# Optimization experiments

Hardware: AMD Instinct MI355X
Metric: run time of the kernel (lower is better)

## Reference

```python
import jax, jax.numpy as jnp
import numpy as np

KS = 3
PAD = 1
N = KS * KS  # 9 sampling points per output location


def setup_inputs() -> dict:
    key = jax.random.key(0)
    k1, k2, k3 = jax.random.split(key, 3)
    b, c, H, W, outc = 4, 128, 64, 64, 128
    x = jax.random.normal(k1, (b, c, H, W), jnp.float32)
    offset = jax.random.normal(k2, (b, 2 * N, H, W), jnp.float32)
    weight = jax.random.normal(k3, (outc, c, KS, KS), jnp.float32) * 0.05
    return {"x": x, "offset": offset, "weight": weight}


def reference(x, offset, weight):
    b, c, H, W = x.shape
    h, w = offset.shape[2], offset.shape[3]
    # reorder interleaved (x,y,x,y,...) offset channels to (all x, all y)
    idx = jnp.concatenate([jnp.arange(0, 2 * N, 2), jnp.arange(1, 2 * N, 2)])
    offset = offset[:, idx]
    # zero padding
    xp = jnp.pad(x, ((0, 0), (0, 0), (PAD, PAD), (PAD, PAD)))
    Hp, Wp = H + 2 * PAD, W + 2 * PAD
    # kernel-relative offsets p_n: [1, 2N, 1, 1]
    r = np.arange(-(KS - 1) // 2, (KS - 1) // 2 + 1)
    pnx, pny = np.meshgrid(r, r, indexing='ij')
    p_n = jnp.asarray(np.concatenate([pnx.flatten(), pny.flatten()]).reshape(1, 2 * N, 1, 1), jnp.float32)
    # base grid p_0: [1, 2N, h, w], coords start at 1 (padded frame)
    p0x, p0y = np.meshgrid(np.arange(1, h + 1), np.arange(1, w + 1), indexing='ij')
    p_0 = jnp.asarray(np.concatenate([np.tile(p0x.reshape(1, 1, h, w), (1, N, 1, 1)),
                                      np.tile(p0y.reshape(1, 1, h, w), (1, N, 1, 1))], axis=1), jnp.float32)
    p = jnp.transpose(p_0 + p_n + offset, (0, 2, 3, 1))  # [b, h, w, 2N]
    px, py = p[..., :N], p[..., N:]
    fx, fy = jnp.floor(px), jnp.floor(py)
    # 4 corner integer coords, clamped to padded image
    q_lt_x = jnp.clip(fx, 0, Hp - 1).astype(jnp.int32)
    q_lt_y = jnp.clip(fy, 0, Wp - 1).astype(jnp.int32)
    q_rb_x = jnp.clip(fx + 1, 0, Hp - 1).astype(jnp.int32)
    q_rb_y = jnp.clip(fy + 1, 0, Wp - 1).astype(jnp.int32)
    # out-of-range mask: snap p to floor(p) there (matches original, incl. zero grad thru floor)
    mask_x = jax.lax.stop_gradient(((px < PAD) | (px > Hp - 1 - PAD)).astype(px.dtype))
    mask_y = jax.lax.stop_gradient(((py < PAD) | (py > Wp - 1 - PAD)).astype(py.dtype))
    px = px * (1 - mask_x) + fx * mask_x
    py = py * (1 - mask_y) + fy * mask_y
    px = jnp.clip(px, 0, Hp - 1)
    py = jnp.clip(py, 0, Wp - 1)
    qltx = q_lt_x.astype(px.dtype); qlty = q_lt_y.astype(px.dtype)
    qrbx = q_rb_x.astype(px.dtype); qrby = q_rb_y.astype(px.dtype)
    # bilinear weights: [b, h, w, N]
    g_lt = (1 + (qltx - px)) * (1 + (qlty - py))
    g_rb = (1 - (qrbx - px)) * (1 - (qrby - py))
    g_lb = (1 + (qltx - px)) * (1 - (qrby - py))
    g_rt = (1 - (qrbx - px)) * (1 + (qlty - py))

    xv = xp.reshape(b, c, Hp * Wp)

    def gather(qx, qy):
        lin = (qx * Wp + qy).reshape(b, 1, h * w * N)
        g = jnp.take_along_axis(xv, jnp.broadcast_to(lin, (b, c, h * w * N)), axis=2)
        return g.reshape(b, c, h, w, N)

    x_off = (g_lt[:, None] * gather(q_lt_x, q_lt_y)
             + g_rb[:, None] * gather(q_rb_x, q_rb_y)
             + g_lb[:, None] * gather(q_lt_x, q_rb_y)
             + g_rt[:, None] * gather(q_rb_x, q_lt_y))  # [b, c, h, w, N]
    # N = i*ks + j -> out[(h,i),(w,j)]
    xo = x_off.reshape(b, c, h, w, KS, KS).transpose(0, 1, 2, 4, 3, 5).reshape(b, c, h * KS, w * KS)
    out = jax.lax.conv_general_dilated(xo, weight, window_strides=(KS, KS), padding='VALID',
                                       dimension_numbers=('NCHW', 'OIHW', 'NCHW'))
    return out
```

## Files before the change

### kernel.cpp

```cpp
#include <hip/hip_runtime.h>


typedef __bf16  v8bf16 __attribute__((ext_vector_type(8)));
typedef __bf16  bf16x2 __attribute__((ext_vector_type(2)));
typedef float   f32x4  __attribute__((ext_vector_type(4)));
typedef float   f32x16 __attribute__((ext_vector_type(16)));
typedef unsigned short ushort4v __attribute__((ext_vector_type(4)));
typedef _Float16 half4v __attribute__((ext_vector_type(4)));

#define CIN  128
#define NPT  9
#define KTOT 1152
#define OC   128
#define PX   32
#define NDESC (NPT * PX)
#define KSTEPS 36
#define KSC  12
#define LDBc 392
#define KS32 72
#define KSC32 24
#define LDR32 392

#define PB_WFRAG 72
#define PB_XPOSE 1024
#define PB_ZERO  2048
#define PB_TOTAL (PB_WFRAG + PB_XPOSE + PB_ZERO)

__device__ __forceinline__ uint4 desc_make(const float* __restrict__ off,
                                           int b, int i, int j, int tap) {
    float ox = off[(((b * 18) + 2 * tap) << 12) + (i << 6) + j];
    float oy = off[(((b * 18) + 2 * tap + 1) << 12) + (i << 6) + j];
    float px = (float)(i + tap / 3) + ox;
    float py = (float)(j + tap % 3) + oy;
    float fx = floorf(px), fy = floorf(py);
    int qltx = (int)fminf(fmaxf(fx, 0.f), 65.f);
    int qlty = (int)fminf(fmaxf(fy, 0.f), 65.f);
    int qrbx = (int)fminf(fmaxf(fx + 1.f, 0.f), 65.f);
    int qrby = (int)fminf(fmaxf(fy + 1.f, 0.f), 65.f);
    if (px < 1.f || px > 64.f) px = fx;
    if (py < 1.f || py > 64.f) py = fy;
    px = fminf(fmaxf(px, 0.f), 65.f);
    py = fminf(fmaxf(py, 0.f), 65.f);
    float wxl = 1.f + (float)qltx - px;
    float wxr = 1.f - ((float)qrbx - px);
    float wyl = 1.f + (float)qlty - py;
    float wyr = 1.f - ((float)qrby - py);
    float g[4] = { wxl * wyl, wxr * wyr, wxl * wyr, wxr * wyl };
    int qx[4] = { qltx, qrbx, qltx, qrbx };
    int qy[4] = { qlty, qrby, qrby, qlty };
    unsigned short idx[4];
    half4v gh;
    #pragma unroll
    for (int cr = 0; cr < 4; ++cr) {
        bool inb = (qx[cr] >= 1) && (qx[cr] <= 64) && (qy[cr] >= 1) && (qy[cr] <= 64);
        idx[cr] = inb ? (unsigned short)((qx[cr] - 1) * 64 + (qy[cr] - 1)) : 0;
        gh[cr]  = inb ? (_Float16)g[cr] : (_Float16)0.f;
    }
    uint4 rec;
    rec.x = (unsigned)idx[0] | ((unsigned)idx[1] << 16);
    rec.y = (unsigned)idx[2] | ((unsigned)idx[3] << 16);
    __builtin_memcpy(&rec.z, &gh, 8);
    return rec;
}

__global__ __launch_bounds__(256) void prep_kernel(
    const float* __restrict__ x, const float* __restrict__ w,
    __bf16* __restrict__ wfrag, __bf16* __restrict__ xt,
    float* __restrict__ out)
{
    __shared__ float tile[64][33];
    const int bid = blockIdx.x;
    const int tid = threadIdx.x;

    if (bid < PB_WFRAG) {
        int t = bid * 256 + tid;
        int lane = t & 63;
        int ks   = (t >> 6) % KS32;
        int ot4  = t / (KS32 * 64);
        int o    = ot4 * 32 + (lane & 31);
        v8bf16 frag;
        #pragma unroll
        for (int e = 0; e < 8; ++e) {
            int k   = ks * 16 + ((lane >> 5) * 8) + e;
            int tap = k >> 7, c = k & 127;
            frag[e] = (__bf16)w[(size_t)o * KTOT + c * NPT + tap];
        }
        *(v8bf16*)(wfrag + (size_t)t * 8) = frag;
    } else if (bid < PB_WFRAG + PB_XPOSE) {
        const int bidx = bid - PB_WFRAG;
        const int b   = bidx >> 8;
        const int hw0 = ((bidx >> 2) & 63) * 64;
        const int c0  = (bidx & 3) * 32;
        #pragma unroll
        for (int r = 0; r < 8; ++r) {
            int c_l  = (tid >> 6) + r * 4;
            int hw_l = tid & 63;
            tile[hw_l][c_l] = x[((size_t)(b * CIN + c0 + c_l) << 12) + hw0 + hw_l];
        }
        __syncthreads();
        #pragma unroll
        for (int r = 0; r < 8; ++r) {
            int hw_l = (tid >> 5) + r * 8;
            int c_l  = tid & 31;
            xt[((size_t)(b * 4096 + hw0 + hw_l)) * CIN + c0 + c_l] = (__bf16)tile[hw_l][c_l];
        }
    } else {
        int t = (bid - PB_WFRAG - PB_XPOSE) * 256 + tid;
        f32x4 z = {0.f, 0.f, 0.f, 0.f};
        *(f32x4*)(out + (size_t)t * 4) = z;
    }
}

__global__ __launch_bounds__(256) void splitk_kernel(
    const float* __restrict__ off, const __bf16* __restrict__ xt,
    const __bf16* __restrict__ wfrag, float* __restrict__ out)
{
    __shared__ __align__(16) __bf16 Bt[PX][LDR32];
    __shared__ __align__(16) uint4 sDesc[96];

    const int bidx = blockIdx.x;
    const int b    = (bidx & 7) >> 1;
    const int sub  = ((bidx >> 3) << 1) | (bidx & 1);
    const int kh3  = sub % 3;
    const int rem  = sub / 3;
    const int i    = rem >> 1;
    const int j0   = (rem & 1) * PX;
    const int tid  = threadIdx.x;

    const int tap0 = kh3 * 3;
    const int l  = tid & 63;
    const int wv = tid >> 6;

    const __bf16* xtb = xt + (((size_t)b << 12) * CIN);

    if (tid < 96) {
        int tt = tid >> 5, p = tid & 31;
        sDesc[tid] = desc_make(off, b, i, j0 + p, tap0 + tt);
    }
    __syncthreads();

    {
        const int q  = l >> 4;
        const int ll = l & 15;
        const __bf16* base = xtb + 8 * ll;

        uint4 qd[6];
        int   pp[6], tt[6];
        #pragma unroll
        for (int m = 0; m < 6; ++m) {
            int dl = wv * 24 + m * 4 + q;
            tt[m] = dl >> 5;
            pp[m] = dl & 31;
            qd[m] = sDesc[dl];
        }

        #pragma unroll
        for (int h = 0; h < 2; ++h) {
            uint4  v[3][4];
            half4v gh[3];
            #pragma unroll
            for (int m = 0; m < 3; ++m) {
                uint4 qm = qd[h * 3 + m];
                unsigned int zz[2] = { qm.z, qm.w };
                __builtin_memcpy(&gh[m], &zz, 8);
                unsigned short idx[4] = {
                    (unsigned short)(qm.x & 0xffff), (unsigned short)(qm.x >> 16),
                    (unsigned short)(qm.y & 0xffff), (unsigned short)(qm.y >> 16) };
                #pragma unroll
                for (int cr = 0; cr < 4; ++cr)
                    v[m][cr] = *(const uint4*)(base + (size_t)idx[cr] * CIN);
            }
            #pragma unroll
            for (int m = 0; m < 3; ++m) {
                float s[8] = {0.f,0.f,0.f,0.f,0.f,0.f,0.f,0.f};
                #pragma unroll
                for (int cr = 0; cr < 4; ++cr) {
                    float gf = (float)gh[m][cr];
                    unsigned int dw[4] = { v[m][cr].x, v[m][cr].y, v[m][cr].z, v[m][cr].w };
                    #pragma unroll
                    for (int e = 0; e < 4; ++e) {
                        float clo, chi;
                        unsigned int lo = dw[e] << 16, hi = dw[e] & 0xffff0000u;
                        __builtin_memcpy(&clo, &lo, 4);
                        __builtin_memcpy(&chi, &hi, 4);
                        s[2 * e]     += gf * clo;
                        s[2 * e + 1] += gf * chi;
                    }
                }
                v8bf16 pr;
                #pragma unroll
                for (int e = 0; e < 8; ++e) pr[e] = (__bf16)s[e];
                int mm = h * 3 + m;
                *(v8bf16*)&Bt[pp[mm]][tt[mm] * CIN + 8 * ll] = pr;
            }
        }
    }
    __syncthreads();

    f32x16 acc = {0.f,0.f,0.f,0.f,0.f,0.f,0.f,0.f,0.f,0.f,0.f,0.f,0.f,0.f,0.f,0.f};
    const __bf16* brow = &Bt[l & 31][(l >> 5) * 8];
    const __bf16* warow = wfrag + (((size_t)wv * KS32 + kh3 * KSC32) * 64 + l) * 8;

    #pragma unroll 6
    for (int ks = 0; ks < KSC32; ++ks) {
        v8bf16 afrag = *(const v8bf16*)(warow + (size_t)ks * 64 * 8);
        v8bf16 bfrag = *(const v8bf16*)(brow + ks * 16);
        acc = __builtin_amdgcn_mfma_f32_32x32x16_bf16(afrag, bfrag, acc, 0, 0, 0);
    }

    {
        int obase = wv * 32 + 4 * (l >> 5);
        float* opb = out + (((size_t)(b * OC + obase)) << 12) + (i << 6) + j0 + (l & 31);
        #pragma unroll
        for (int reg = 0; reg < 16; ++reg) {
            int oo = (reg & 3) + 8 * (reg >> 2);
            unsafeAtomicAdd(opb + ((size_t)oo << 12), acc[reg]);
        }
    }
}

__global__ __launch_bounds__(512, 8) void deform_fused_kernel(
    const float* __restrict__ x, const float* __restrict__ off,
    const float* __restrict__ w, const __bf16* __restrict__ wfrag,
    const __bf16* __restrict__ xt, float* __restrict__ out, int mode)
{
    __shared__ __align__(16) __bf16 Bt[PX][LDBc];
    __shared__ __align__(8)  unsigned short sIdxP[NDESC][4];
    __shared__ __align__(8)  _Float16      sGP[NDESC][4];

    const int bidx = blockIdx.x;
    const int b   = bidx >> 8;
    const int i   = (bidx >> 2) & 63;
    const int j0  = ((bidx >> 1) & 1) * PX;
    const int oh  = bidx & 1;
    const int tid = threadIdx.x;

    if (tid < NDESC) {
        int k = tid >> 5, p = tid & 31;
        int j = j0 + p;
        float ox = off[(((b * 18) + 2 * k) * 64 + i) * 64 + j];
        float oy = off[(((b * 18) + 2 * k + 1) * 64 + i) * 64 + j];
        float px = (float)(i + k / 3) + ox;
        float py = (float)(j + k % 3) + oy;
        float fx = floorf(px), fy = floorf(py);
        int qltx = (int)fminf(fmaxf(fx, 0.f), 65.f);
        int qlty = (int)fminf(fmaxf(fy, 0.f), 65.f);
        int qrbx = (int)fminf(fmaxf(fx + 1.f, 0.f), 65.f);
        int qrby = (int)fminf(fmaxf(fy + 1.f, 0.f), 65.f);
        if (px < 1.f || px > 64.f) px = fx;
        if (py < 1.f || py > 64.f) py = fy;
        px = fminf(fmaxf(px, 0.f), 65.f);
        py = fminf(fmaxf(py, 0.f), 65.f);
        float wxl = 1.f + (float)qltx - px;
        float wxr = 1.f - ((float)qrbx - px);
        float wyl = 1.f + (float)qlty - py;
        float wyr = 1.f - ((float)qrby - py);
        float g[4] = { wxl * wyl, wxr * wyr, wxl * wyr, wxr * wyl };
        int qx[4] = { qltx, qrbx, qltx, qrbx };
        int qy[4] = { qlty, qrby, qrby, qlty };
        #pragma unroll
        for (int cr = 0; cr < 4; ++cr) {
            bool inb = (qx[cr] >= 1) && (qx[cr] <= 64) && (qy[cr] >= 1) && (qy[cr] <= 64);
            sIdxP[tid][cr] = inb ? (unsigned short)((qx[cr] - 1) * 64 + (qy[cr] - 1)) : 0;
            sGP[tid][cr]   = inb ? (_Float16)g[cr] : (_Float16)0.f;
        }
    }
    __syncthreads();

    const int l    = tid & 63;
    const int wv   = tid >> 6;
    const int ot   = oh * 4 + (wv & 3);
    const int ph   = wv >> 2;
    const int quad = l >> 4;
    const int lr   = l & 15;

    f32x4 acc = {0.f, 0.f, 0.f, 0.f};
    const __bf16* xtb = xt + ((size_t)b * 4096) * CIN;
    const float*  xb  = x + ((size_t)b * CIN << 12);
    const __bf16* brow = &Bt[ph * 16 + lr][quad * 8];

    for (int t = 0; t < 3; ++t) {
        if (mode == 2) {
            #pragma unroll 4
            for (int dd = 0; dd < KSC; ++dd) {
                int dl = wv * KSC + dd;
                int tap_l = dl >> 5, p = dl & 31;
                int d = t * 96 + dl;
                ushort4v id = *(const ushort4v*)&sIdxP[d][0];
                half4v   gh = *(const half4v*)&sGP[d][0];
                float s0 = 0.f, s1 = 0.f;
                #pragma unroll
                for (int cr = 0; cr < 4; ++cr) {
                    unsigned int v = *(const unsigned int*)(xtb + (size_t)id[cr] * CIN + 2 * l);
                    float c0v, c1v;
                    unsigned int lo = v << 16, hi = v & 0xffff0000u;
                    __builtin_memcpy(&c0v, &lo, 4);
                    __builtin_memcpy(&c1v, &hi, 4);
                    float gf = (float)gh[cr];
                    s0 += gf * c0v;
                    s1 += gf * c1v;
                }
                bf16x2 pr = { (__bf16)s0, (__bf16)s1 };
                *(bf16x2*)&Bt[p][tap_l * CIN + 2 * l] = pr;
            }
        } else {
            for (int dd = 0; dd < KSC; ++dd) {
                int dl = wv * KSC + dd;
                int tap_l = dl >> 5, p = dl & 31;
                int d = t * 96 + dl;
                ushort4v id = *(const ushort4v*)&sIdxP[d][0];
                half4v   gh = *(const half4v*)&sGP[d][0];
                float s0 = 0.f, s1 = 0.f;
                #pragma unroll
                for (int cr = 0; cr < 4; ++cr) {
                    float gf = (float)gh[cr];
                    s0 += gf * xb[((size_t)(2 * l) << 12) + id[cr]];
                    s1 += gf * xb[((size_t)(2 * l + 1) << 12) + id[cr]];
                }
                bf16x2 pr = { (__bf16)s0, (__bf16)s1 };
                *(bf16x2*)&Bt[p][tap_l * CIN + 2 * l] = pr;
            }
        }
        __syncthreads();

        #pragma unroll 4
        for (int ks = 0; ks < KSC; ++ks) {
            int ks_g = t * KSC + ks;
            v8bf16 bfrag = *(const v8bf16*)(brow + ks * 32);
            v8bf16 afrag;
            if (mode >= 1) {
                afrag = *(const v8bf16*)(wfrag + (((size_t)ot * KSTEPS + ks_g) * 64 + l) * 8);
            } else {
                int o = ot * 16 + lr;
                #pragma unroll
                for (int e = 0; e < 8; ++e) {
                    int k = ks_g * 32 + quad * 8 + e;
                    int tap = k >> 7, c = k & 127;
                    afrag[e] = (__bf16)w[(size_t)o * KTOT + c * NPT + tap];
                }
            }
            acc = __builtin_amdgcn_mfma_f32_16x16x32_bf16(afrag, bfrag, acc, 0, 0, 0);
        }
        if (t < 2) __syncthreads();
    }

    {
        int obase = ot * 16 + quad * 4;
        float* op = out + (((size_t)(b * OC + obase)) << 12) + (i << 6) + j0 + ph * 16 + lr;
        #pragma unroll
        for (int r = 0; r < 4; ++r)
            op[(size_t)r << 12] = acc[r];
    }
}

__global__ __launch_bounds__(256) void wfrag_kernel(const float* __restrict__ w,
                                                    __bf16* __restrict__ wfrag) {
    int t = blockIdx.x * 256 + threadIdx.x;
    if (t >= 8 * KSTEPS * 64) return;
    int lane = t & 63;
    int ks   = (t >> 6) % KSTEPS;
    int ot   = t / (KSTEPS * 64);
    int o    = ot * 16 + (lane & 15);
    v8bf16 frag;
    #pragma unroll
    for (int e = 0; e < 8; ++e) {
        int k   = ks * 32 + (lane >> 4) * 8 + e;
        int tap = k >> 7, c = k & 127;
        frag[e] = (__bf16)w[(size_t)o * KTOT + c * NPT + tap];
    }
    *(v8bf16*)(wfrag + (size_t)t * 8) = frag;
}

__global__ __launch_bounds__(256) void xpose_kernel(const float* __restrict__ x,
                                                    __bf16* __restrict__ xt) {
    __shared__ float tile[64][33];
    const int bidx = blockIdx.x;
    const int b   = bidx >> 8;
    const int hw0 = ((bidx >> 2) & 63) * 64;
    const int c0  = (bidx & 3) * 32;
    const int tid = threadIdx.x;
    #pragma unroll
    for (int r = 0; r < 8; ++r) {
        int c_l  = (tid >> 6) + r * 4;
        int hw_l = tid & 63;
        tile[hw_l][c_l] = x[((size_t)(b * CIN + c0 + c_l) << 12) + hw0 + hw_l];
    }
    __syncthreads();
    #pragma unroll
    for (int r = 0; r < 8; ++r) {
        int hw_l = (tid >> 5) + r * 8;
        int c_l  = tid & 31;
        xt[((size_t)(b * 4096 + hw0 + hw_l)) * CIN + c0 + c_l] = (__bf16)tile[hw_l][c_l];
    }
}

extern "C" void kernel_launch(void* const* d_in, const int* in_sizes, int n_in,
                              void* d_out, int out_size, void* d_ws, size_t ws_size,
                              hipStream_t stream) {
    const float* x   = (const float*)d_in[0];
    const float* off = (const float*)d_in[1];
    const float* w   = (const float*)d_in[2];
    float* out = (float*)d_out;

    const size_t wfrag_bytes = (size_t)OC * KTOT * sizeof(__bf16);
    const size_t xt_bytes    = (size_t)4 * 4096 * CIN * sizeof(__bf16);

    int mode = 0;
    if (ws_size >= wfrag_bytes + xt_bytes) mode = 3;
    else if (ws_size >= wfrag_bytes) mode = 1;

    __bf16* wfrag = (__bf16*)d_ws;
    __bf16* xt    = (__bf16*)((char*)d_ws + wfrag_bytes);

    if (mode == 3) {
        prep_kernel<<<PB_TOTAL, 256, 0, stream>>>(x, w, wfrag, xt, out);
        splitk_kernel<<<1536, 256, 0, stream>>>(off, xt, wfrag, out);
    } else {
        if (mode >= 1)
            wfrag_kernel<<<(8 * KSTEPS * 64 + 255) / 256, 256, 0, stream>>>(w, wfrag);
        deform_fused_kernel<<<4 * 64 * 2 * 2, 512, 0, stream>>>(x, off, w, wfrag, xt, out, mode);
    }
}
```

Baseline: 94.03 us.

## Replace split-K atomic kernel with full-K per-block loop and direct stores

The split-K kernel, which split the three kernel rows across 1536 blocks and combined them with atomic adds into a pre-zeroed output, is replaced by a full-K kernel of 512 blocks. Each block loops over the three tap rows, building the sampled tile and accumulating the MFMA results in registers, then writes the output with plain stores. This removes the output zeroing pass in the prep kernel and the atomic traffic. In exchange there are a third as many blocks, so less parallelism to hide gather latency, and the gather and MFMA phases are serialized within each block by extra barriers.

Result: faster. 84.75 us (-9.9%).

```diff
diff --git a/kernel.cpp b/kernel.cpp
--- a/kernel.cpp
+++ b/kernel.cpp
@@ -23,8 +23,7 @@
 
 #define PB_WFRAG 72
 #define PB_XPOSE 1024
-#define PB_ZERO  2048
-#define PB_TOTAL (PB_WFRAG + PB_XPOSE + PB_ZERO)
+#define PB_TOTAL (PB_WFRAG + PB_XPOSE)
 
 __device__ __forceinline__ uint4 desc_make(const float* __restrict__ off,
                                            int b, int i, int j, int tap) {
@@ -65,8 +64,7 @@
 
 __global__ __launch_bounds__(256) void prep_kernel(
     const float* __restrict__ x, const float* __restrict__ w,
-    __bf16* __restrict__ wfrag, __bf16* __restrict__ xt,
-    float* __restrict__ out)
+    __bf16* __restrict__ wfrag, __bf16* __restrict__ xt)
 {
     __shared__ float tile[64][33];
     const int bid = blockIdx.x;
@@ -86,7 +84,7 @@
             frag[e] = (__bf16)w[(size_t)o * KTOT + c * NPT + tap];
         }
         *(v8bf16*)(wfrag + (size_t)t * 8) = frag;
-    } else if (bid < PB_WFRAG + PB_XPOSE) {
+    } else {
         const int bidx = bid - PB_WFRAG;
         const int b   = bidx >> 8;
         const int hw0 = ((bidx >> 2) & 63) * 64;
@@ -104,108 +102,104 @@
             int c_l  = tid & 31;
             xt[((size_t)(b * 4096 + hw0 + hw_l)) * CIN + c0 + c_l] = (__bf16)tile[hw_l][c_l];
         }
-    } else {
-        int t = (bid - PB_WFRAG - PB_XPOSE) * 256 + tid;
-        f32x4 z = {0.f, 0.f, 0.f, 0.f};
-        *(f32x4*)(out + (size_t)t * 4) = z;
-    }
-}
-
-__global__ __launch_bounds__(256) void splitk_kernel(
+    }
+}
+
+__global__ __launch_bounds__(256) void fullk_kernel(
     const float* __restrict__ off, const __bf16* __restrict__ xt,
     const __bf16* __restrict__ wfrag, float* __restrict__ out)
 {
     __shared__ __align__(16) __bf16 Bt[PX][LDR32];
-    __shared__ __align__(16) uint4 sDesc[96];
+    __shared__ __align__(16) uint4 sDesc[NDESC];
 
     const int bidx = blockIdx.x;
     const int b    = (bidx & 7) >> 1;
     const int sub  = ((bidx >> 3) << 1) | (bidx & 1);
-    const int kh3  = sub % 3;
-    const int rem  = sub / 3;
-    const int i    = rem >> 1;
-    const int j0   = (rem & 1) * PX;
+    const int i    = sub >> 1;
+    const int j0   = (sub & 1) * PX;
     const int tid  = threadIdx.x;
 
-    const int tap0 = kh3 * 3;
     const int l  = tid & 63;
     const int wv = tid >> 6;
 
     const __bf16* xtb = xt + (((size_t)b << 12) * CIN);
 
-    if (tid < 96) {
-        int tt = tid >> 5, p = tid & 31;
-        sDesc[tid] = desc_make(off, b, i, j0 + p, tap0 + tt);
+    {
+        sDesc[tid] = desc_make(off, b, i, j0 + (tid & 31), tid >> 5);
+        if (tid < 32) sDesc[256 + tid] = desc_make(off, b, i, j0 + tid, 8);
     }
     __syncthreads();
 
-    {
-        const int q  = l >> 4;
-        const int ll = l & 15;
-        const __bf16* base = xtb + 8 * ll;
-
-        uint4 qd[6];
-        int   pp[6], tt[6];
-        #pragma unroll
-        for (int m = 0; m < 6; ++m) {
-            int dl = wv * 24 + m * 4 + q;
-            tt[m] = dl >> 5;
-            pp[m] = dl & 31;
-            qd[m] = sDesc[dl];
-        }
-
-        #pragma unroll
-        for (int h = 0; h < 2; ++h) {
-            uint4  v[3][4];
-            half4v gh[3];
+    f32x16 acc = {0.f,0.f,0.f,0.f,0.f,0.f,0.f,0.f,0.f,0.f,0.f,0.f,0.f,0.f,0.f,0.f};
+    const __bf16* brow  = &Bt[l & 31][(l >> 5) * 8];
+    const __bf16* warow = wfrag + (((size_t)wv * KS32) * 64 + l) * 8;
+
+    const int q  = l >> 4;
+    const int ll = l & 15;
+    const __bf16* gbase = xtb + 8 * ll;
+
+    for (int t = 0; t < 3; ++t) {
+        {
+            uint4 qd[6];
+            int   pp[6], tt[6];
             #pragma unroll
-            for (int m = 0; m < 3; ++m) {
-                uint4 qm = qd[h * 3 + m];
-                unsigned int zz[2] = { qm.z, qm.w };
-                __builtin_memcpy(&gh[m], &zz, 8);
-                unsigned short idx[4] = {
-                    (unsigned short)(qm.x & 0xffff), (unsigned short)(qm.x >> 16),
-                    (unsigned short)(qm.y & 0xffff), (unsigned short)(qm.y >> 16) };
+            for (int m = 0; m < 6; ++m) {
+                int dl = wv * 24 + m * 4 + q;
+                tt[m] = dl >> 5;
+                pp[m] = dl & 31;
+                qd[m] = sDesc[t * 96 + dl];
+            }
+
+            #pragma unroll
+            for (int h = 0; h < 2; ++h) {
+                uint4  v[3][4];
+                half4v gh[3];
                 #pragma unroll
-                for (int cr = 0; cr < 4; ++cr)
-                    v[m][cr] = *(const uint4*)(base + (size_t)idx[cr] * CIN);
+                for (int m = 0; m < 3; ++m) {
+                    uint4 qm = qd[h * 3 + m];
+                    unsigned int zz[2] = { qm.z, qm.w };
+                    __builtin_memcpy(&gh[m], &zz, 8);
+                    unsigned short idx[4] = {
+                        (unsigned short)(qm.x & 0xffff), (unsigned short)(qm.x >> 16),
+                        (unsigned short)(qm.y & 0xffff), (unsigned short)(qm.y >> 16) };
+                    #pragma unroll
+                    for (int cr = 0; cr < 4; ++cr)
+                        v[m][cr] = *(const uint4*)(gbase + (size_t)idx[cr] * CIN);
+                }
+                #pragma unroll
+                for (int m = 0; m < 3; ++m) {
+                    float s[8] = {0.f,0.f,0.f,0.f,0.f,0.f,0.f,0.f};
+                    #pragma unroll
+                    for (int cr = 0; cr < 4; ++cr) {
+                        float gf = (float)gh[m][cr];
+                        unsigned int dw[4] = { v[m][cr].x, v[m][cr].y, v[m][cr].z, v[m][cr].w };
+                        #pragma unroll
+                        for (int e = 0; e < 4; ++e) {
+                            float clo, chi;
+                            unsigned int lo = dw[e] << 16, hi = dw[e] & 0xffff0000u;
+                            __builtin_memcpy(&clo, &lo, 4);
+                            __builtin_memcpy(&chi, &hi, 4);
+                            s[2 * e]     += gf * clo;
+                            s[2 * e + 1] += gf * chi;
+                        }
+                    }
+                    v8bf16 pr;
+                    #pragma unroll
+                    for (int e = 0; e < 8; ++e) pr[e] = (__bf16)s[e];
+                    int mm = h * 3 + m;
+                    *(v8bf16*)&Bt[pp[mm]][tt[mm] * CIN + 8 * ll] = pr;
+                }
             }
-            #pragma unroll
-            for (int m = 0; m < 3; ++m) {
-                float s[8] = {0.f,0.f,0.f,0.f,0.f,0.f,0.f,0.f};
-                #pragma unroll
-                for (int cr = 0; cr < 4; ++cr) {
-                    float gf = (float)gh[m][cr];
-                    unsigned int dw[4] = { v[m][cr].x, v[m][cr].y, v[m][cr].z, v[m][cr].w };
-                    #pragma unroll
-                    for (int e = 0; e < 4; ++e) {
-                        float clo, chi;
-                        unsigned int lo = dw[e] << 16, hi = dw[e] & 0xffff0000u;
-                        __builtin_memcpy(&clo, &lo, 4);
-                        __builtin_memcpy(&chi, &hi, 4);
-                        s[2 * e]     += gf * clo;
-                        s[2 * e + 1] += gf * chi;
-                    }
-                }
-                v8bf16 pr;
-                #pragma unroll
-                for (int e = 0; e < 8; ++e) pr[e] = (__bf16)s[e];
-                int mm = h * 3 + m;
-                *(v8bf16*)&Bt[pp[mm]][tt[mm] * CIN + 8 * ll] = pr;
-            }
-        }
-    }
-    __syncthreads();
-
-    f32x16 acc = {0.f,0.f,0.f,0.f,0.f,0.f,0.f,0.f,0.f,0.f,0.f,0.f,0.f,0.f,0.f,0.f};
-    const __bf16* brow = &Bt[l & 31][(l >> 5) * 8];
-    const __bf16* warow = wfrag + (((size_t)wv * KS32 + kh3 * KSC32) * 64 + l) * 8;
-
-    #pragma unroll 6
-    for (int ks = 0; ks < KSC32; ++ks) {
-        v8bf16 afrag = *(const v8bf16*)(warow + (size_t)ks * 64 * 8);
-        v8bf16 bfrag = *(const v8bf16*)(brow + ks * 16);
-        acc = __builtin_amdgcn_mfma_f32_32x32x16_bf16(afrag, bfrag, acc, 0, 0, 0);
+        }
+        __syncthreads();
+
+        #pragma unroll 6
+        for (int ks = 0; ks < KSC32; ++ks) {
+            v8bf16 afrag = *(const v8bf16*)(warow + (size_t)(t * KSC32 + ks) * 64 * 8);
+            v8bf16 bfrag = *(const v8bf16*)(brow + ks * 16);
+            acc = __builtin_amdgcn_mfma_f32_32x32x16_bf16(afrag, bfrag, acc, 0, 0, 0);
+        }
+        if (t < 2) __syncthreads();
     }
 
     {
@@ -214,7 +208,7 @@
         #pragma unroll
         for (int reg = 0; reg < 16; ++reg) {
             int oo = (reg & 3) + 8 * (reg >> 2);
-            unsafeAtomicAdd(opb + ((size_t)oo << 12), acc[reg]);
+            opb[(size_t)oo << 12] = acc[reg];
         }
     }
 }
@@ -413,8 +407,8 @@
     __bf16* xt    = (__bf16*)((char*)d_ws + wfrag_bytes);
 
     if (mode == 3) {
-        prep_kernel<<<PB_TOTAL, 256, 0, stream>>>(x, w, wfrag, xt, out);
-        splitk_kernel<<<1536, 256, 0, stream>>>(off, xt, wfrag, out);
+        prep_kernel<<<PB_TOTAL, 256, 0, stream>>>(x, w, wfrag, xt);
+        fullk_kernel<<<512, 256, 0, stream>>>(off, xt, wfrag, out);
     } else {
         if (mode >= 1)
             wfrag_kernel<<<(8 * KSTEPS * 64 + 255) / 256, 256, 0, stream>>>(w, wfrag);
```
